# Performance work log

Measured on AMD Instinct MI355X. Metric: run time of the kernel, lower is better.

Reference implementation:

```python
import jax, jax.numpy as jnp
import numpy as np
from jax import lax

B, S, H = 1, 2048, 1024
NH, NKV, HD = 16, 4, 64        # heads, kv heads, head_dim = H // NH
I = 3584                        # intermediate size
E, TOPK = 8, 2                  # experts, top-k routing
EPS = 1e-5
THETA = 1e6


def setup_inputs() -> dict:
    key = jax.random.key(0)
    ks = jax.random.split(key, 12)
    sc = 0.02
    return {
        "hidden_states": jax.random.normal(ks[0], (B, S, H), jnp.float32),
        "position_ids": jnp.broadcast_to(jnp.arange(S, dtype=jnp.int32), (B, S)),
        "wq": jax.random.normal(ks[1], (H, NH * HD), jnp.float32) * sc,
        "wk": jax.random.normal(ks[2], (H, NKV * HD), jnp.float32) * sc,
        "wv": jax.random.normal(ks[3], (H, NKV * HD), jnp.float32) * sc,
        "wo": jax.random.normal(ks[4], (NH * HD, H), jnp.float32) * sc,
        "input_norm_w": jnp.ones((H,), jnp.float32),
        "post_norm_w": jnp.ones((H,), jnp.float32),
        "gate_w": jax.random.normal(ks[5], (H, E), jnp.float32) * sc,
        "w1": jax.random.normal(ks[6], (E, H, I), jnp.float32) * sc,
        "w3": jax.random.normal(ks[7], (E, H, I), jnp.float32) * sc,
        "w2": jax.random.normal(ks[8], (E, I, H), jnp.float32) * sc,
    }


def _rmsnorm(x, w):
    var = jnp.mean(jnp.square(x), axis=-1, keepdims=True)
    return x * lax.rsqrt(var + EPS) * w


def _rope(q, k, position_ids):
    # q: [B,S,NH,HD], k: [B,S,NKV,HD]
    inv_freq = 1.0 / (THETA ** (jnp.arange(0, HD, 2, dtype=jnp.float32) / HD))
    freqs = position_ids.astype(jnp.float32)[..., None] * inv_freq  # [B,S,HD/2]
    emb = jnp.concatenate([freqs, freqs], axis=-1)                  # [B,S,HD]
    cos = jnp.cos(emb)[:, :, None, :]
    sin = jnp.sin(emb)[:, :, None, :]

    def rot_half(x):
        x1, x2 = jnp.split(x, 2, axis=-1)
        return jnp.concatenate([-x2, x1], axis=-1)

    return q * cos + rot_half(q) * sin, k * cos + rot_half(k) * sin


def _attention(x, position_ids, wq, wk, wv, wo):
    b, s, _ = x.shape
    q = (x @ wq).reshape(b, s, NH, HD)
    k = (x @ wk).reshape(b, s, NKV, HD)
    v = (x @ wv).reshape(b, s, NKV, HD)
    q, k = _rope(q, k, position_ids)
    groups = NH // NKV
    k = jnp.repeat(k, groups, axis=2)  # [B,S,NH,HD]
    v = jnp.repeat(v, groups, axis=2)
    scale = HD ** -0.5
    scores = jnp.einsum("bqhd,bkhd->bhqk", q, k) * scale
    causal = jnp.tril(jnp.ones((s, s), dtype=bool))
    scores = jnp.where(causal[None, None], scores, jnp.finfo(scores.dtype).min)
    probs = jax.nn.softmax(scores, axis=-1)
    out = jnp.einsum("bhqk,bkhd->bqhd", probs, v).reshape(b, s, NH * HD)
    return out @ wo


def _moe(x, gate_w, w1, w3, w2):
    b, s, h = x.shape
    xt = x.reshape(b * s, h)
    logits = xt @ gate_w                      # [T,E]
    probs = jax.nn.softmax(logits, axis=-1)
    top_w, top_i = lax.top_k(probs, TOPK)     # [T,K]
    top_w = top_w / jnp.sum(top_w, axis=-1, keepdims=True)
    out = jnp.zeros_like(xt)
    for e in range(E):
        we = jnp.sum(jnp.where(top_i == e, top_w, 0.0), axis=-1)   # [T]
        h_e = jax.nn.silu(xt @ w1[e]) * (xt @ w3[e])               # [T,I]
        out = out + we[:, None] * (h_e @ w2[e])
    return out.reshape(b, s, h), logits


def reference(hidden_states, position_ids, wq, wk, wv, wo,
              input_norm_w, post_norm_w, gate_w, w1, w3, w2):
    # MixtralDecoderLayer: norm -> GQA attn -> residual -> norm -> MoE -> residual
    attn_out = _attention(_rmsnorm(hidden_states, input_norm_w),
                          position_ids, wq, wk, wv, wo)
    h = hidden_states + attn_out
    moe_out, _router_logits = _moe(_rmsnorm(h, post_norm_w), gate_w, w1, w3, w2)
    return h + moe_out
```

## Files before the change

kernel.cpp:

```cpp
#include <hip/hip_runtime.h>
#include <math.h>


typedef unsigned short u16;
typedef unsigned int u32;
typedef __attribute__((ext_vector_type(8))) short s16x8;
typedef __attribute__((ext_vector_type(8))) _Float16 f16x8;
typedef __attribute__((ext_vector_type(4))) float f32x4;

#define S_LEN 2048
#define HDIM  1024
#define NHEAD 16
#define NKVH  4
#define HD    64
#define ISZ   3584
#define NEXP  8
#define NSLOT 4096
#define EPS_F 1e-5f
#define NEG_INF -1e30f
#define LOG2E 1.44269504f

__device__ __forceinline__ float bf2f(u16 u) {
    union { u32 i; float f; } c; c.i = ((u32)u) << 16; return c.f;
}
__device__ __forceinline__ u16 f2bf(float f) {
    union { float f; u32 i; } c; c.f = f;
    u32 r = (c.i + 0x7fffu + ((c.i >> 16) & 1u)) >> 16;
    return (u16)r;
}
__device__ __forceinline__ u16 f2h_bits(float f) {
    union { _Float16 h; u16 u; } c; c.h = (_Float16)f; return c.u;
}
__device__ __forceinline__ void async16(const u16* g, u16* l) {
    __builtin_amdgcn_global_load_lds(
        (const __attribute__((address_space(1))) void*)g,
        (__attribute__((address_space(3))) void*)l, 16, 0, 0);
}

__global__ void k_zero_ints(int* __restrict__ p, int n) {
    int i = blockIdx.x * blockDim.x + threadIdx.x;
    if (i < n) p[i] = 0;
}

__global__ __launch_bounds__(256)
void k_rmsnorm_bf(const float* __restrict__ x, const float* __restrict__ w,
                  u16* __restrict__ out) {
    int t = blockIdx.x;
    int tid = threadIdx.x;
    float4 v = ((const float4*)(x + (size_t)t * HDIM))[tid];
    float ss = v.x * v.x + v.y * v.y + v.z * v.z + v.w * v.w;
#pragma unroll
    for (int off = 32; off >= 1; off >>= 1) ss += __shfl_xor(ss, off, 64);
    __shared__ float red[4];
    if ((tid & 63) == 0) red[tid >> 6] = ss;
    __syncthreads();
    float tot = red[0] + red[1] + red[2] + red[3];
    float rstd = rsqrtf(tot * (1.0f / HDIM) + EPS_F);
    float4 wv = ((const float4*)w)[tid];
    uint2 pk;
    pk.x = (u32)f2bf(v.x * rstd * wv.x) | ((u32)f2bf(v.y * rstd * wv.y) << 16);
    pk.y = (u32)f2bf(v.z * rstd * wv.z) | ((u32)f2bf(v.w * rstd * wv.w) << 16);
    ((uint2*)(out + (size_t)t * HDIM))[tid] = pk;
}

__global__ __launch_bounds__(256)
void k_cvt_t(const float* __restrict__ src, u16* __restrict__ dst,
             int R, int C, long long srcZ, long long dstZ) {
    const int z = blockIdx.z;
    src += (size_t)z * srcZ;
    dst += (size_t)z * dstZ;
    const int lane = threadIdx.x & 63, w = threadIdx.x >> 6;
    const int c = blockIdx.x * 64 + lane;
    const int r0 = blockIdx.y * 128 + w * 32;
    float v[32];
#pragma unroll
    for (int i = 0; i < 32; i++) v[i] = src[(size_t)(r0 + i) * C + c];
#pragma unroll
    for (int g = 0; g < 4; g++) {
        uint4 pk;
        pk.x = (u32)f2bf(v[g * 8 + 0]) | ((u32)f2bf(v[g * 8 + 1]) << 16);
        pk.y = (u32)f2bf(v[g * 8 + 2]) | ((u32)f2bf(v[g * 8 + 3]) << 16);
        pk.z = (u32)f2bf(v[g * 8 + 4]) | ((u32)f2bf(v[g * 8 + 5]) << 16);
        pk.w = (u32)f2bf(v[g * 8 + 6]) | ((u32)f2bf(v[g * 8 + 7]) << 16);
        *(uint4*)(&dst[(size_t)c * R + r0 + g * 8]) = pk;
    }
}

__device__ __forceinline__ void stage32(const u16* __restrict__ A,
                                        const u16* __restrict__ Bt, int K,
                                        int rowA0, int rowAmax, int n0, int kc,
                                        u16* buf, int wid, int sr, int sc) {
#pragma unroll
    for (int t = 0; t < 2; t++) {
        int row = wid * 32 + t * 16 + sr;
        int ck = (sc ^ (row & 3)) << 3;
        int ra = rowA0 + row;
        if (ra > rowAmax) ra = rowAmax;
        u16* ldsA = buf + (wid * 32 + t * 16) * 32;
        async16(A + (size_t)ra * K + kc + ck, ldsA);
        async16(Bt + (size_t)(n0 + row) * K + kc + ck, ldsA + 4096);
    }
}

__device__ __forceinline__ void stage_w13(const u16* __restrict__ A,
                                          const u16* __restrict__ B1,
                                          const u16* __restrict__ B3,
                                          int rowA0, int n0, int kc,
                                          u16* buf, int wid, int sr, int sc) {
    int row = wid * 16 + sr;
    int ck = (sc ^ (row & 3)) << 3;
    int ra = rowA0 + row;
    if (ra > NSLOT - 1) ra = NSLOT - 1;
    u16* dst = buf + (wid * 16) * 32;
    async16(A  + (size_t)ra * HDIM + kc + ck, dst);
    async16(B1 + (size_t)(n0 + row) * HDIM + kc + ck, dst + 4096);
    async16(B3 + (size_t)(n0 + row) * HDIM + kc + ck, dst + 8192);
}

__device__ __forceinline__ void gemm128_dbuf(
    const u16* __restrict__ A, const u16* __restrict__ Bt, int K,
    int kbeg, int kend, int rowA0, int rowAmax, int n0,
    u16* lds, f32x4 acc[4][4]) {
    const int tid = threadIdx.x;
    const int lane = tid & 63, wid = tid >> 6;
    const int sr = lane >> 2, sc = lane & 3;
    const int ln = lane & 15, q = lane >> 4;
    const int wm = wid >> 1, wn = wid & 1;
    stage32(A, Bt, K, rowA0, rowAmax, n0, kbeg, lds, wid, sr, sc);
    int pp = 0;
    for (int kc = kbeg; kc < kend; kc += 32) {
        u16* cur = lds + pp * 8192;
        u16* nxt = lds + (pp ^ 1) * 8192;
        pp ^= 1;
        __syncthreads();
        if (kc + 32 < kend)
            stage32(A, Bt, K, rowA0, rowAmax, n0, kc + 32, nxt, wid, sr, sc);
        s16x8 af[4], bfv[4];
#pragma unroll
        for (int i = 0; i < 4; i++) {
            int ar = wm * 64 + i * 16 + ln;
            af[i] = *(const s16x8*)(cur + ar * 32 + ((q ^ (ar & 3)) << 3));
            int br = wn * 64 + i * 16 + ln;
            bfv[i] = *(const s16x8*)(cur + 4096 + br * 32 + ((q ^ (br & 3)) << 3));
        }
#pragma unroll
        for (int i = 0; i < 4; i++)
#pragma unroll
            for (int j = 0; j < 4; j++)
                acc[i][j] = __builtin_amdgcn_mfma_f32_16x16x32_bf16(
                    af[i], bfv[j], acc[i][j], 0, 0, 0);
    }
}

__global__ __launch_bounds__(256, 2)
void k_gemm_bt(const u16* __restrict__ A, const u16* __restrict__ Bt,
               int M, int N, int K, int mode,
               float* __restrict__ F0, float* __restrict__ F1,
               const float* __restrict__ RES, u16* __restrict__ O16) {
    __shared__ u16 lds[16384];
    const int m0 = blockIdx.y * 128, n0 = blockIdx.x * 128;
    f32x4 acc[4][4];
#pragma unroll
    for (int i = 0; i < 4; i++)
#pragma unroll
        for (int j = 0; j < 4; j++) acc[i][j] = (f32x4){0.f, 0.f, 0.f, 0.f};
    gemm128_dbuf(A, Bt, K, 0, K, m0, M - 1, n0, lds, acc);
    const int lane = threadIdx.x & 63, wid = threadIdx.x >> 6;
    const int ln = lane & 15, q = lane >> 4, wm = wid >> 1, wn = wid & 1;
#pragma unroll
    for (int i = 0; i < 4; i++) {
#pragma unroll
        for (int r = 0; r < 4; r++) {
            int m = m0 + wm * 64 + i * 16 + q * 4 + r;
#pragma unroll
            for (int j = 0; j < 4; j++) {
                int n = n0 + wn * 64 + j * 16 + ln;
                float v = acc[i][j][r];
                if (mode == 0) {
                    F0[(size_t)m * N + n] = v;
                } else if (mode == 1) {
                    O16[(size_t)m * N + n] = f2bf(v);
                } else if (mode == 2) {
                    F0[(size_t)m * N + n] = v + RES[(size_t)m * N + n];
                } else {
                    if (n < 1024)       F0[(size_t)m * 1024 + n] = v;
                    else if (n < 1280)  F1[(size_t)m * 256 + (n - 1024)] = v;
                    else                O16[(size_t)m * 256 + (n - 1280)] = f2h_bits(v);
                }
            }
        }
    }
}

__global__ __launch_bounds__(512, 4)
void k_moe_w13(const u16* __restrict__ Xg, const u16* __restrict__ W1T,
               const u16* __restrict__ W3T, u16* __restrict__ He,
               const int* __restrict__ offs, const int* __restrict__ mlist,
               const int* __restrict__ nitems) {
    __shared__ u16 lds[24576];
    const int NB = ISZ / 128;
    const int tot = nitems[0] * NB;
    const int tid = threadIdx.x;
    const int lane = tid & 63, wid = tid >> 6;
    const int sr = lane >> 2, sc = lane & 3;
    const int ln = lane & 15, q = lane >> 4;
    const int wm = wid >> 2, wn = wid & 3;
    for (int it = blockIdx.x; it < tot; it += gridDim.x) {
        const int mi = it / NB, nb = it - mi * NB;
        const int em = mlist[mi];
        const int e = em >> 8, mb = em & 255;
        const int base = offs[e], cnt = offs[e + 1] - base;
        const int m0 = mb * 128, n0 = nb * 128;
        const int rowA0 = base + m0;
        const u16* B1 = W1T + (size_t)e * ISZ * HDIM;
        const u16* B3 = W3T + (size_t)e * ISZ * HDIM;
        f32x4 acc1[4][2], acc3[4][2];
#pragma unroll
        for (int i = 0; i < 4; i++)
#pragma unroll
            for (int j = 0; j < 2; j++) {
                acc1[i][j] = (f32x4){0.f, 0.f, 0.f, 0.f};
                acc3[i][j] = (f32x4){0.f, 0.f, 0.f, 0.f};
            }
        __syncthreads();
        stage_w13(Xg, B1, B3, rowA0, n0, 0, lds, wid, sr, sc);
        int pp = 0;
        for (int kc = 0; kc < HDIM; kc += 32) {
            u16* cur = lds + pp * 12288;
            u16* nxt = lds + (pp ^ 1) * 12288;
            pp ^= 1;
            __syncthreads();
            if (kc + 32 < HDIM)
                stage_w13(Xg, B1, B3, rowA0, n0, kc + 32, nxt, wid, sr, sc);
            s16x8 af[4], b1f[2], b3f[2];
#pragma unroll
            for (int i = 0; i < 4; i++) {
                int ar = wm * 64 + i * 16 + ln;
                af[i] = *(const s16x8*)(cur + ar * 32 + ((q ^ (ar & 3)) << 3));
            }
#pragma unroll
            for (int j = 0; j < 2; j++) {
                int br = wn * 32 + j * 16 + ln;
                int bo = br * 32 + ((q ^ (br & 3)) << 3);
                b1f[j] = *(const s16x8*)(cur + 4096 + bo);
                b3f[j] = *(const s16x8*)(cur + 8192 + bo);
            }
#pragma unroll
            for (int i = 0; i < 4; i++)
#pragma unroll
                for (int j = 0; j < 2; j++) {
                    acc1[i][j] = __builtin_amdgcn_mfma_f32_16x16x32_bf16(
                        af[i], b1f[j], acc1[i][j], 0, 0, 0);
                    acc3[i][j] = __builtin_amdgcn_mfma_f32_16x16x32_bf16(
                        af[i], b3f[j], acc3[i][j], 0, 0, 0);
                }
        }
#pragma unroll
        for (int i = 0; i < 4; i++) {
#pragma unroll
            for (int r = 0; r < 4; r++) {
                int mloc = wm * 64 + i * 16 + q * 4 + r;
                if (m0 + mloc >= cnt) continue;
                size_t row = (size_t)(base + m0 + mloc);
#pragma unroll
                for (int j = 0; j < 2; j++) {
                    int n = n0 + wn * 32 + j * 16 + ln;
                    float v1 = acc1[i][j][r];
                    float v3 = acc3[i][j][r];
                    float s = v1 / (1.0f + expf(-v1));
                    He[row * ISZ + n] = f2bf(s * v3);
                }
            }
        }
    }
}

__global__ __launch_bounds__(256, 3)
void k_moe_w2(const u16* __restrict__ He, const u16* __restrict__ W2T,
              float* __restrict__ OA, float* __restrict__ OB,
              const int* __restrict__ offs, const int* __restrict__ mlist,
              const int* __restrict__ nitems) {
    __shared__ u16 lds[16384];
    const int tot = nitems[0] * 16;
    const int lane = threadIdx.x & 63, wid = threadIdx.x >> 6;
    const int ln = lane & 15, q = lane >> 4, wm = wid >> 1, wn = wid & 1;
    for (int it = blockIdx.x; it < tot; it += gridDim.x) {
        const int mi = it >> 4, rr = it & 15;
        const int nb = rr & 7, half = rr >> 3;
        const int em = mlist[mi];
        const int e = em >> 8, mb = em & 255;
        const int base = offs[e], cnt = offs[e + 1] - base;
        const int m0 = mb * 128, n0 = nb * 128;
        const u16* Bt = W2T + (size_t)e * HDIM * ISZ;
        f32x4 acc[4][4];
#pragma unroll
        for (int i = 0; i < 4; i++)
#pragma unroll
            for (int j = 0; j < 4; j++) acc[i][j] = (f32x4){0.f, 0.f, 0.f, 0.f};
        __syncthreads();
        gemm128_dbuf(He, Bt, ISZ, half * (ISZ / 2), (half + 1) * (ISZ / 2),
                     base + m0, NSLOT - 1, n0, lds, acc);
        float* F0 = half ? OB : OA;
#pragma unroll
        for (int i = 0; i < 4; i++) {
#pragma unroll
            for (int r = 0; r < 4; r++) {
                int mloc = wm * 64 + i * 16 + q * 4 + r;
                if (m0 + mloc >= cnt) continue;
                size_t row = (size_t)(base + m0 + mloc);
#pragma unroll
                for (int j = 0; j < 4; j++) {
                    int n = n0 + wn * 64 + j * 16 + ln;
                    F0[row * HDIM + n] = acc[i][j][r];
                }
            }
        }
    }
}

__global__ __launch_bounds__(256)
void k_rope_cvt(const float* __restrict__ q, const float* __restrict__ k,
                const int* __restrict__ pos, u16* __restrict__ qb2,
                u16* __restrict__ kb2) {
    int id = blockIdx.x * blockDim.x + threadIdx.x;
    int d = id & 31;
    int hh = (id >> 5) % (NHEAD + NKVH);
    int s = id / ((NHEAD + NKVH) * 32);
    float p = (float)pos[s];
    float inv = exp2f(-((float)(2 * d) / (float)HD) * log2f(1.0e6f));
    float ang = p * inv;
    float c = cosf(ang), sn = sinf(ang);
    const float* sp; u16* dp;
    if (hh < NHEAD) {
        sp = q + (size_t)s * (NHEAD * HD) + hh * HD;
        dp = qb2 + (size_t)s * (NHEAD * HD) + hh * HD;
    } else {
        sp = k + (size_t)s * (NKVH * HD) + (hh - NHEAD) * HD;
        dp = kb2 + (size_t)s * (NKVH * HD) + (hh - NHEAD) * HD;
    }
    float x1 = sp[d], x2 = sp[d + 32];
    dp[d]      = f2h_bits(x1 * c - x2 * sn);
    dp[d + 32] = f2h_bits(x2 * c + x1 * sn);
}

__global__ __launch_bounds__(256)
void k_attn_mfma(const u16* __restrict__ qb, const u16* __restrict__ kb,
                 const u16* __restrict__ vb, u16* __restrict__ ob) {
    __shared__ u16 Qs[64 * 64];
    __shared__ u16 Ks[64 * 64];
    __shared__ u16 Vt[64 * 64];
    __shared__ u16 Ps[64 * 64];
    const int qt = blockIdx.x, h = blockIdx.y, kvh = h >> 2;
    const int tid = threadIdx.x, lane = tid & 63, w = tid >> 6;
    const int ln = lane & 15, quad = lane >> 4;

#pragma unroll
    for (int p = 0; p < 2; p++) {
        int r = p * 32 + (tid >> 3), c = tid & 7;
        uint4 v = *(const uint4*)(qb + (size_t)(qt * 64 + r) * (NHEAD * HD) +
                                  h * HD + c * 8);
        *(uint4*)&Qs[r * 64 + ((c ^ (r & 7)) << 3)] = v;
    }

    float m_[4], l_[4];
    f32x4 Oa[4];
#pragma unroll
    for (int r = 0; r < 4; r++) { m_[r] = NEG_INF; l_[r] = 0.0f; }
#pragma unroll
    for (int nt = 0; nt < 4; nt++) Oa[nt] = (f32x4){0.f, 0.f, 0.f, 0.f};

    for (int kt = 0; kt <= qt; kt++) {
        __syncthreads();
#pragma unroll
        for (int p = 0; p < 2; p++) {
            int r = p * 32 + (tid >> 3), c = tid & 7;
            uint4 v = *(const uint4*)(kb + (size_t)(kt * 64 + r) * (NKVH * HD) +
                                      kvh * HD + c * 8);
            *(uint4*)&Ks[r * 64 + ((c ^ (r & 7)) << 3)] = v;
        }
        {
            int s = tid & 63;
#pragma unroll
            for (int half = 0; half < 2; half++) {
                int d0 = w * 16 + half * 8;
                uint4 v = *(const uint4*)(vb + (size_t)(kt * 64 + s) * (NKVH * HD) +
                                          kvh * HD + d0);
                u16 a[8];
                a[0] = (u16)(v.x & 0xffff); a[1] = (u16)(v.x >> 16);
                a[2] = (u16)(v.y & 0xffff); a[3] = (u16)(v.y >> 16);
                a[4] = (u16)(v.z & 0xffff); a[5] = (u16)(v.z >> 16);
                a[6] = (u16)(v.w & 0xffff); a[7] = (u16)(v.w >> 16);
#pragma unroll
                for (int j = 0; j < 8; j++) {
                    int d = d0 + j;
                    Vt[d * 64 + (((s >> 3) ^ (d & 7)) << 3) + (s & 7)] = a[j];
                }
            }
        }
        __syncthreads();

        f32x4 sc[4];
#pragma unroll
        for (int nt = 0; nt < 4; nt++) sc[nt] = (f32x4){0.f, 0.f, 0.f, 0.f};
#pragma unroll
        for (int ks = 0; ks < 2; ks++) {
            int arow = 16 * w + ln;
            f16x8 af = *(const f16x8*)&Qs[arow * 64 +
                                          (((ks * 4 + quad) ^ (arow & 7)) << 3)];
#pragma unroll
            for (int nt = 0; nt < 4; nt++) {
                int brow = nt * 16 + ln;
                f16x8 bf = *(const f16x8*)&Ks[brow * 64 +
                                              (((ks * 4 + quad) ^ (brow & 7)) << 3)];
                sc[nt] = __builtin_amdgcn_mfma_f32_16x16x32_f16(af, bf, sc[nt],
                                                                0, 0, 0);
            }
        }

        const bool diag = (kt == qt);
        float mt[4];
#pragma unroll
        for (int r = 0; r < 4; r++) {
            int qrow = quad * 4 + r + 16 * w;
#pragma unroll
            for (int nt = 0; nt < 4; nt++) {
                float s = sc[nt][r] * 0.125f;
                if (diag && (nt * 16 + ln) > qrow) s = NEG_INF;
                sc[nt][r] = s;
            }
            mt[r] = fmaxf(fmaxf(sc[0][r], sc[1][r]), fmaxf(sc[2][r], sc[3][r]));
        }
#pragma unroll
        for (int off = 8; off >= 1; off >>= 1)
#pragma unroll
            for (int r = 0; r < 4; r++)
                mt[r] = fmaxf(mt[r], __shfl_xor(mt[r], off, 64));

        float rs[4];
#pragma unroll
        for (int r = 0; r < 4; r++) {
            float mn = fmaxf(m_[r], mt[r]);
            float al = exp2f((m_[r] - mn) * LOG2E);
            m_[r] = mn;
            float acc0 = 0.0f;
#pragma unroll
            for (int nt = 0; nt < 4; nt++) {
                float pv = exp2f((sc[nt][r] - mn) * LOG2E);
                sc[nt][r] = pv;
                acc0 += pv;
            }
            rs[r] = acc0;
            l_[r] *= al;
#pragma unroll
            for (int nt = 0; nt < 4; nt++) Oa[nt][r] *= al;
        }
#pragma unroll
        for (int off = 8; off >= 1; off >>= 1)
#pragma unroll
            for (int r = 0; r < 4; r++) rs[r] += __shfl_xor(rs[r], off, 64);
#pragma unroll
        for (int r = 0; r < 4; r++) l_[r] += rs[r];

#pragma unroll
        for (int r = 0; r < 4; r++) {
            int row = 16 * w + quad * 4 + r;
#pragma unroll
            for (int nt = 0; nt < 4; nt++) {
                int ch = nt * 2 + (ln >> 3);
                Ps[row * 64 + ((ch ^ (row & 7)) << 3) + (ln & 7)] =
                    f2h_bits(sc[nt][r]);
            }
        }
        __syncthreads();

#pragma unroll
        for (int ks = 0; ks < 2; ks++) {
            int arow = 16 * w + ln;
            f16x8 pf = *(const f16x8*)&Ps[arow * 64 +
                                          (((ks * 4 + quad) ^ (arow & 7)) << 3)];
#pragma unroll
            for (int nt = 0; nt < 4; nt++) {
                int vrow = nt * 16 + ln;
                f16x8 vf = *(const f16x8*)&Vt[vrow * 64 +
                                              (((ks * 4 + quad) ^ (vrow & 7)) << 3)];
                Oa[nt] = __builtin_amdgcn_mfma_f32_16x16x32_f16(pf, vf, Oa[nt],
                                                                0, 0, 0);
            }
        }
    }

#pragma unroll
    for (int r = 0; r < 4; r++) {
        float inv = 1.0f / l_[r];
        int sg = qt * 64 + 16 * w + quad * 4 + r;
#pragma unroll
        for (int nt = 0; nt < 4; nt++) {
            int d = nt * 16 + ln;
            ob[(size_t)sg * HDIM + h * HD + d] = f2bf(Oa[nt][r] * inv);
        }
    }
}

__global__ __launch_bounds__(64)
void k_gate(const float* __restrict__ Hst, const float* __restrict__ PW,
            const float* __restrict__ GW, int* __restrict__ cnt,
            int* __restrict__ top_i, float* __restrict__ top_w) {
    int t = blockIdx.x;
    int lane = threadIdx.x;
    const float* hrow = Hst + (size_t)t * HDIM;
    float ss = 0.0f;
    float acc[NEXP] = {};
    for (int hh = lane; hh < HDIM; hh += 64) {
        float hv = hrow[hh];
        ss += hv * hv;
        float xw = hv * PW[hh];
        const float* g = GW + (size_t)hh * NEXP;
#pragma unroll
        for (int e = 0; e < NEXP; e++) acc[e] += xw * g[e];
    }
#pragma unroll
    for (int off = 32; off >= 1; off >>= 1) {
        ss += __shfl_xor(ss, off, 64);
#pragma unroll
        for (int e = 0; e < NEXP; e++) acc[e] += __shfl_xor(acc[e], off, 64);
    }
    if (lane == 0) {
        float rstd = rsqrtf(ss * (1.0f / HDIM) + EPS_F);
        int e0 = 0;
        for (int e = 1; e < NEXP; e++) if (acc[e] > acc[e0]) e0 = e;
        int e1 = (e0 == 0) ? 1 : 0;
        for (int e = 0; e < NEXP; e++)
            if (e != e0 && acc[e] > acc[e1]) e1 = e;
        float w0 = 1.0f / (1.0f + expf((acc[e1] - acc[e0]) * rstd));
        top_i[t * 2 + 0] = e0; top_i[t * 2 + 1] = e1;
        top_w[t * 2 + 0] = w0; top_w[t * 2 + 1] = 1.0f - w0;
        atomicAdd(&cnt[e0], 1);
        atomicAdd(&cnt[e1], 1);
    }
}

__global__ void k_prefix(const int* __restrict__ cnt, int* __restrict__ offs,
                         int* __restrict__ cur, int* __restrict__ mlist,
                         int* __restrict__ nitems) {
    if (blockIdx.x == 0 && threadIdx.x == 0) {
        int a = 0, idx = 0;
        for (int e = 0; e < NEXP; e++) {
            offs[e] = a; cur[e] = a;
            int c = cnt[e];
            int nmb = (c + 127) >> 7;
            for (int mb = 0; mb < nmb; mb++) mlist[idx++] = (e << 8) | mb;
            a += c;
        }
        offs[NEXP] = a;
        nitems[0] = idx;
    }
}

__global__ __launch_bounds__(256)
void k_fill(const int* __restrict__ top_i, int* __restrict__ cur,
            int* __restrict__ idxg, int* __restrict__ slot) {
    int t = blockIdx.x * blockDim.x + threadIdx.x;
    if (t >= S_LEN) return;
#pragma unroll
    for (int kk = 0; kk < 2; kk++) {
        int e = top_i[t * 2 + kk];
        int p = atomicAdd(&cur[e], 1);
        idxg[p] = t;
        slot[t * 2 + kk] = p;
    }
}

__global__ __launch_bounds__(256)
void k_gather(const u16* __restrict__ xnb, const int* __restrict__ idxg,
              u16* __restrict__ Xg) {
    int p = blockIdx.x;
    int t = idxg[p];
    const uint2* s = (const uint2*)(xnb + (size_t)t * HDIM);
    uint2* d = (uint2*)(Xg + (size_t)p * HDIM);
    d[threadIdx.x] = s[threadIdx.x];
}

__global__ __launch_bounds__(256)
void k_combine2(const float* __restrict__ OA, const float* __restrict__ OB,
                const int* __restrict__ slot, const float* __restrict__ top_w,
                float* __restrict__ out) {
    int t = blockIdx.x, tid = threadIdx.x;
    int s0 = slot[t * 2], s1 = slot[t * 2 + 1];
    float w0 = top_w[t * 2], w1 = top_w[t * 2 + 1];
    float4 a0 = ((const float4*)(OA + (size_t)s0 * HDIM))[tid];
    float4 b0 = ((const float4*)(OB + (size_t)s0 * HDIM))[tid];
    float4 a1 = ((const float4*)(OA + (size_t)s1 * HDIM))[tid];
    float4 b1 = ((const float4*)(OB + (size_t)s1 * HDIM))[tid];
    float4* o = (float4*)(out + (size_t)t * HDIM);
    float4 c = o[tid];
    c.x += w0 * (a0.x + b0.x) + w1 * (a1.x + b1.x);
    c.y += w0 * (a0.y + b0.y) + w1 * (a1.y + b1.y);
    c.z += w0 * (a0.z + b0.z) + w1 * (a1.z + b1.z);
    c.w += w0 * (a0.w + b0.w) + w1 * (a1.w + b1.w);
    o[tid] = c;
}

extern "C" void kernel_launch(void* const* d_in, const int* in_sizes, int n_in,
                              void* d_out, int out_size, void* d_ws,
                              size_t ws_size, hipStream_t stream) {
    (void)in_sizes; (void)n_in; (void)out_size; (void)ws_size;
    const float* hidden = (const float*)d_in[0];
    const int*   pos    = (const int*)d_in[1];
    const float* wq     = (const float*)d_in[2];
    const float* wk     = (const float*)d_in[3];
    const float* wv     = (const float*)d_in[4];
    const float* wo     = (const float*)d_in[5];
    const float* innw   = (const float*)d_in[6];
    const float* postnw = (const float*)d_in[7];
    const float* gatew  = (const float*)d_in[8];
    const float* w1     = (const float*)d_in[9];
    const float* w3     = (const float*)d_in[10];
    const float* w2     = (const float*)d_in[11];
    float* out = (float*)d_out;

    u16* w1t  = (u16*)d_ws;
    u16* w3t  = w1t + (size_t)NEXP * ISZ * HDIM;
    u16* w2t  = w3t + (size_t)NEXP * ISZ * HDIM;
    u16* qkvt = w2t + (size_t)NEXP * ISZ * HDIM;
    u16* wot  = qkvt + (size_t)1536 * HDIM;
    u16* xnb  = wot + (size_t)HDIM * HDIM;
    float* qbuf = (float*)(xnb + (size_t)S_LEN * HDIM);
    float* kbuf = qbuf + (size_t)S_LEN * HDIM;
    u16* vb16   = (u16*)(kbuf + (size_t)S_LEN * NKVH * HD);
    u16* qb2    = vb16 + (size_t)S_LEN * NKVH * HD;
    u16* kb2    = qb2 + (size_t)S_LEN * HDIM;
    u16* attnb  = kb2 + (size_t)S_LEN * NKVH * HD;
    float* oexpA = qbuf;
    u16* Xg  = attnb + (size_t)S_LEN * HDIM;
    u16* hg3 = Xg + (size_t)NSLOT * HDIM;
    u16* he  = hg3 + (size_t)NSLOT * ISZ;
    float* oexpB = (float*)(he + (size_t)NSLOT * ISZ);
    int* ib  = (int*)(oexpB + (size_t)NSLOT * HDIM);
    int*   cnt   = ib;
    int*   offs  = ib + 16;
    int*   cur   = ib + 32;
    int*   top_i = ib + 64;
    int*   slot  = ib + 64 + 4096;
    int*   idxg  = ib + 64 + 8192;
    float* top_w = (float*)(ib + 64 + 12288);
    int*   mlist = ib + 64 + 16384;
    int*   nitems = ib + 64 + 16384 + 128;

    const long long HI = (long long)HDIM * ISZ;

    k_zero_ints<<<1, 64, 0, stream>>>(cnt, 64);
    k_rmsnorm_bf<<<S_LEN, 256, 0, stream>>>(hidden, innw, xnb);

    k_cvt_t<<<dim3(16, 8, 1), 256, 0, stream>>>(wq, qkvt, 1024, 1024, 0, 0);
    k_cvt_t<<<dim3(4, 8, 1), 256, 0, stream>>>(wk, qkvt + (size_t)1024 * 1024, 1024, 256, 0, 0);
    k_cvt_t<<<dim3(4, 8, 1), 256, 0, stream>>>(wv, qkvt + (size_t)1280 * 1024, 1024, 256, 0, 0);
    k_cvt_t<<<dim3(16, 8, 1), 256, 0, stream>>>(wo, wot, 1024, 1024, 0, 0);
    k_cvt_t<<<dim3(56, 8, NEXP), 256, 0, stream>>>(w1, w1t, 1024, 3584, HI, HI);
    k_cvt_t<<<dim3(56, 8, NEXP), 256, 0, stream>>>(w3, w3t, 1024, 3584, HI, HI);
    k_cvt_t<<<dim3(16, 28, NEXP), 256, 0, stream>>>(w2, w2t, 3584, 1024, HI, HI);

    k_gemm_bt<<<dim3(12, 16), 256, 0, stream>>>(xnb, qkvt, 2048, 1536, 1024, 3,
                                                qbuf, kbuf, nullptr, vb16);
    k_rope_cvt<<<(S_LEN * (NHEAD + NKVH) * 32) / 256, 256, 0, stream>>>(
        qbuf, kbuf, pos, qb2, kb2);
    k_attn_mfma<<<dim3(32, 16), 256, 0, stream>>>(qb2, kb2, vb16, attnb);
    k_gemm_bt<<<dim3(8, 16), 256, 0, stream>>>(attnb, wot, 2048, 1024, 1024, 2,
                                               out, nullptr, hidden, nullptr);
    k_rmsnorm_bf<<<S_LEN, 256, 0, stream>>>(out, postnw, xnb);
    k_gate<<<S_LEN, 64, 0, stream>>>(out, postnw, gatew, cnt, top_i, top_w);
    k_prefix<<<1, 1, 0, stream>>>(cnt, offs, cur, mlist, nitems);
    k_fill<<<S_LEN / 256, 256, 0, stream>>>(top_i, cur, idxg, slot);
    k_gather<<<NSLOT, 256, 0, stream>>>(xnb, idxg, Xg);

    k_moe_w13<<<dim3(512), 512, 0, stream>>>(Xg, w1t, w3t, he, offs, mlist,
                                             nitems);
    k_moe_w2<<<dim3(1024), 256, 0, stream>>>(he, w2t, oexpA, oexpB, offs,
                                             mlist, nitems);
    k_combine2<<<S_LEN, 256, 0, stream>>>(oexpA, oexpB, slot, top_w, out);
}
```

Before: 828.0 us.

## Switch GEMM mainloops to triple-buffered LDS with vmcnt waits and single barrier

```diff
diff --git a/kernel.cpp b/kernel.cpp
--- a/kernel.cpp
+++ b/kernel.cpp
@@ -117,7 +117,7 @@
     async16(B3 + (size_t)(n0 + row) * HDIM + kc + ck, dst + 8192);
 }
 
-__device__ __forceinline__ void gemm128_dbuf(
+__device__ __forceinline__ void gemm128_tbuf(
     const u16* __restrict__ A, const u16* __restrict__ Bt, int K,
     int kbeg, int kend, int rowA0, int rowAmax, int n0,
     u16* lds, f32x4 acc[4][4]) {
@@ -127,14 +127,20 @@
     const int ln = lane & 15, q = lane >> 4;
     const int wm = wid >> 1, wn = wid & 1;
     stage32(A, Bt, K, rowA0, rowAmax, n0, kbeg, lds, wid, sr, sc);
+    if (kbeg + 32 < kend)
+        stage32(A, Bt, K, rowA0, rowAmax, n0, kbeg + 32, lds + 8192,
+                wid, sr, sc);
     int pp = 0;
     for (int kc = kbeg; kc < kend; kc += 32) {
         u16* cur = lds + pp * 8192;
-        u16* nxt = lds + (pp ^ 1) * 8192;
-        pp ^= 1;
-        __syncthreads();
-        if (kc + 32 < kend)
-            stage32(A, Bt, K, rowA0, rowAmax, n0, kc + 32, nxt, wid, sr, sc);
+        if (kc + 32 < kend) asm volatile("s_waitcnt vmcnt(4)" ::: "memory");
+        else                asm volatile("s_waitcnt vmcnt(0)" ::: "memory");
+        __builtin_amdgcn_s_barrier();
+        if (kc + 64 < kend) {
+            int pn = pp + 2; if (pn >= 3) pn -= 3;
+            stage32(A, Bt, K, rowA0, rowAmax, n0, kc + 64, lds + pn * 8192,
+                    wid, sr, sc);
+        }
         s16x8 af[4], bfv[4];
 #pragma unroll
         for (int i = 0; i < 4; i++) {
@@ -149,22 +155,23 @@
             for (int j = 0; j < 4; j++)
                 acc[i][j] = __builtin_amdgcn_mfma_f32_16x16x32_bf16(
                     af[i], bfv[j], acc[i][j], 0, 0, 0);
-    }
-}
-
-__global__ __launch_bounds__(256, 2)
+        pp = (pp + 1 == 3) ? 0 : pp + 1;
+    }
+}
+
+__global__ __launch_bounds__(256, 3)
 void k_gemm_bt(const u16* __restrict__ A, const u16* __restrict__ Bt,
                int M, int N, int K, int mode,
                float* __restrict__ F0, float* __restrict__ F1,
                const float* __restrict__ RES, u16* __restrict__ O16) {
-    __shared__ u16 lds[16384];
+    __shared__ u16 lds[24576];
     const int m0 = blockIdx.y * 128, n0 = blockIdx.x * 128;
     f32x4 acc[4][4];
 #pragma unroll
     for (int i = 0; i < 4; i++)
 #pragma unroll
         for (int j = 0; j < 4; j++) acc[i][j] = (f32x4){0.f, 0.f, 0.f, 0.f};
-    gemm128_dbuf(A, Bt, K, 0, K, m0, M - 1, n0, lds, acc);
+    gemm128_tbuf(A, Bt, K, 0, K, m0, M - 1, n0, lds, acc);
     const int lane = threadIdx.x & 63, wid = threadIdx.x >> 6;
     const int ln = lane & 15, q = lane >> 4, wm = wid >> 1, wn = wid & 1;
 #pragma unroll
@@ -197,7 +204,7 @@
                const u16* __restrict__ W3T, u16* __restrict__ He,
                const int* __restrict__ offs, const int* __restrict__ mlist,
                const int* __restrict__ nitems) {
-    __shared__ u16 lds[24576];
+    __shared__ u16 lds[36864];
     const int NB = ISZ / 128;
     const int tot = nitems[0] * NB;
     const int tid = threadIdx.x;
@@ -224,14 +231,18 @@
             }
         __syncthreads();
         stage_w13(Xg, B1, B3, rowA0, n0, 0, lds, wid, sr, sc);
+        stage_w13(Xg, B1, B3, rowA0, n0, 32, lds + 12288, wid, sr, sc);
         int pp = 0;
         for (int kc = 0; kc < HDIM; kc += 32) {
             u16* cur = lds + pp * 12288;
-            u16* nxt = lds + (pp ^ 1) * 12288;
-            pp ^= 1;
-            __syncthreads();
-            if (kc + 32 < HDIM)
-                stage_w13(Xg, B1, B3, rowA0, n0, kc + 32, nxt, wid, sr, sc);
+            if (kc + 32 < HDIM) asm volatile("s_waitcnt vmcnt(3)" ::: "memory");
+            else                asm volatile("s_waitcnt vmcnt(0)" ::: "memory");
+            __builtin_amdgcn_s_barrier();
+            if (kc + 64 < HDIM) {
+                int pn = pp + 2; if (pn >= 3) pn -= 3;
+                stage_w13(Xg, B1, B3, rowA0, n0, kc + 64, lds + pn * 12288,
+                          wid, sr, sc);
+            }
             s16x8 af[4], b1f[2], b3f[2];
 #pragma unroll
             for (int i = 0; i < 4; i++) {
@@ -254,6 +265,7 @@
                     acc3[i][j] = __builtin_amdgcn_mfma_f32_16x16x32_bf16(
                         af[i], b3f[j], acc3[i][j], 0, 0, 0);
                 }
+            pp = (pp + 1 == 3) ? 0 : pp + 1;
         }
 #pragma unroll
         for (int i = 0; i < 4; i++) {
@@ -280,7 +292,7 @@
               float* __restrict__ OA, float* __restrict__ OB,
               const int* __restrict__ offs, const int* __restrict__ mlist,
               const int* __restrict__ nitems) {
-    __shared__ u16 lds[16384];
+    __shared__ u16 lds[24576];
     const int tot = nitems[0] * 16;
     const int lane = threadIdx.x & 63, wid = threadIdx.x >> 6;
     const int ln = lane & 15, q = lane >> 4, wm = wid >> 1, wn = wid & 1;
@@ -298,7 +310,7 @@
 #pragma unroll
             for (int j = 0; j < 4; j++) acc[i][j] = (f32x4){0.f, 0.f, 0.f, 0.f};
         __syncthreads();
-        gemm128_dbuf(He, Bt, ISZ, half * (ISZ / 2), (half + 1) * (ISZ / 2),
+        gemm128_tbuf(He, Bt, ISZ, half * (ISZ / 2), (half + 1) * (ISZ / 2),
                      base + m0, NSLOT - 1, n0, lds, acc);
         float* F0 = half ? OB : OA;
 #pragma unroll
@@ -674,7 +686,7 @@
 
     k_moe_w13<<<dim3(512), 512, 0, stream>>>(Xg, w1t, w3t, he, offs, mlist,
                                              nitems);
-    k_moe_w2<<<dim3(1024), 256, 0, stream>>>(he, w2t, oexpA, oexpB, offs,
-                                             mlist, nitems);
+    k_moe_w2<<<dim3(768), 256, 0, stream>>>(he, w2t, oexpA, oexpB, offs,
+                                            mlist, nitems);
     k_combine2<<<S_LEN, 256, 0, stream>>>(oexpA, oexpB, slot, top_w, out);
 }
```

New measurement: 824.5 us. Within noise of the previous version (-0.4%).
